# Kernel tuning notes

Measured on AMD Instinct MI355X. Metric: run time of the kernel, lower is better.

Reference implementation:

```python
import jax, jax.numpy as jnp
import numpy as np

D_MODEL = 1024
N_HEADS = 16
HEAD_DIM = D_MODEL // N_HEADS
SEQ = 2048
BATCH = 2
ROPE_BASE = 10000.0


def rope_cos_sin(seq_len, dim, dtype=jnp.float32):
    inv_freq = 1.0 / (ROPE_BASE ** (jnp.arange(0, dim, 2, dtype=jnp.float32) / dim))
    pos = jnp.arange(seq_len, dtype=jnp.float32)
    freqs = jnp.outer(pos, inv_freq)              # [S, dim/2]
    emb = jnp.concatenate([freqs, freqs], axis=-1)  # [S, dim]
    return jnp.cos(emb).astype(dtype), jnp.sin(emb).astype(dtype)


def rotate_half(x):
    x1, x2 = jnp.split(x, 2, axis=-1)
    return jnp.concatenate([-x2, x1], axis=-1)


def setup_inputs() -> dict:
    key = jax.random.key(0)
    kx, kq, kk, kv, ko = jax.random.split(key, 5)
    x = jax.random.normal(kx, (BATCH, SEQ, D_MODEL), dtype=jnp.float32)
    # causal boolean mask, broadcastable to [B, H, S, S]
    attn_mask = jnp.tril(jnp.ones((SEQ, SEQ), dtype=bool))[None, None]
    s = 1.0 / np.sqrt(D_MODEL)
    Wq = jax.random.normal(kq, (D_MODEL, D_MODEL), dtype=jnp.float32) * s
    Wk = jax.random.normal(kk, (D_MODEL, D_MODEL), dtype=jnp.float32) * s
    Wv = jax.random.normal(kv, (D_MODEL, D_MODEL), dtype=jnp.float32) * s
    Wo = jax.random.normal(ko, (D_MODEL, D_MODEL), dtype=jnp.float32) * s
    return {"x": x, "attn_mask": attn_mask, "Wq": Wq, "Wk": Wk, "Wv": Wv, "Wo": Wo}


def reference(x, attn_mask, Wq, Wk, Wv, Wo):
    B, S, _ = x.shape
    dtype = x.dtype
    # projections (nn.Linear: x @ W.T)
    def split_heads(t):
        return t.reshape(B, S, N_HEADS, HEAD_DIM).transpose(0, 2, 1, 3)  # [B,H,S,Dh]
    q = split_heads(x @ Wq.T)
    k = split_heads(x @ Wk.T)
    v = split_heads(x @ Wv.T)
    # RoPE
    cos, sin = rope_cos_sin(S, HEAD_DIM, dtype)  # [S, Dh]
    cos = cos[None, None]
    sin = sin[None, None]
    q = q * cos + rotate_half(q) * sin
    k = k * cos + rotate_half(k) * sin
    # float mask: 0 where True, finfo.min where False
    neg = jnp.finfo(dtype).min
    float_mask = jnp.where(attn_mask, jnp.zeros((), dtype), jnp.full((), neg, dtype))
    # scaled dot product attention
    scale = 1.0 / np.sqrt(HEAD_DIM)
    scores = jnp.einsum("bhqd,bhkd->bhqk", q, k) * scale + float_mask
    attn = jax.nn.softmax(scores, axis=-1)
    out = jnp.einsum("bhqk,bhkd->bhqd", attn, v)  # [B,H,S,Dh]
    out = out.transpose(0, 2, 1, 3).reshape(B, S, D_MODEL)
    return out @ Wo.T
```

## Files before the change

### kernel.cpp

```cpp
#include <hip/hip_runtime.h>
#include <hip/hip_bf16.h>
#include <math.h>

typedef unsigned short ushort_t;
typedef __attribute__((ext_vector_type(8))) short short8;
typedef __attribute__((ext_vector_type(4))) float f32x4;

#define D_MODEL 1024
#define SEQ     2048
#define NH      16
#define HD      64
#define BATCH   2
#define M_TOTAL (BATCH * SEQ)
#define SCL     0.18033688f
#define HSZ     4194304

__device__ __forceinline__ ushort_t f2bf(float f) {
    __hip_bfloat16 h = __float2bfloat16(f);
    ushort_t u;
    __builtin_memcpy(&u, &h, 2);
    return u;
}
__device__ __forceinline__ unsigned pack2(float a, float b) {
    __hip_bfloat162 h = __float22bfloat162_rn(make_float2(a, b));
    unsigned u;
    __builtin_memcpy(&u, &h, 4);
    return u;
}
__device__ __forceinline__ float fexp2(float x) { return __builtin_amdgcn_exp2f(x); }

typedef const __attribute__((address_space(1))) void* gp_t;
typedef __attribute__((address_space(3))) void* lp_t;
__device__ __forceinline__ void cp16(const void* g, void* l) {
    __builtin_amdgcn_global_load_lds((gp_t)g, (lp_t)l, 16, 0, 0);
}

__global__ __launch_bounds__(256) void prep(
    const float* __restrict__ x,
    const float* __restrict__ w0, const float* __restrict__ w1,
    const float* __restrict__ w2, const float* __restrict__ w3,
    ushort_t* __restrict__ xb, ushort_t* __restrict__ wb,
    float2* __restrict__ tab)
{
    int bid = blockIdx.x;
    if (bid < 4096) {
        size_t e = ((size_t)bid * 256 + threadIdx.x) * 8;
        const float* src;
        ushort_t* dst;
        size_t off;
        if (e < (size_t)HSZ) {
            src = x; dst = xb; off = e;
        } else {
            size_t r = e - HSZ;
            int j = (int)(r >> 20);
            off = r & 1048575u;
            src = (j == 0) ? w0 : (j == 1) ? w1 : (j == 2) ? w2 : w3;
            dst = wb + ((size_t)j << 20);
        }
        float4 a = *(const float4*)&src[off];
        float4 b = *(const float4*)&src[off + 4];
        uint4 u;
        u.x = pack2(a.x, a.y);
        u.y = pack2(a.z, a.w);
        u.z = pack2(b.x, b.y);
        u.w = pack2(b.z, b.w);
        *(uint4*)&dst[off] = u;
    } else {
        int idx = (bid - 4096) * 256 + threadIdx.x;
        int i = idx & 31, s = idx >> 5;
        float invf = powf(10000.0f, -(float)(2 * i) * (1.0f / 64.0f));
        float fr = (float)s * invf;
        float sn, cs;
        sincosf(fr, &sn, &cs);
        tab[idx] = make_float2(cs, sn);
    }
}


#define STAGE(K0, SB) do {                                                   \
    cp16(&A [(size_t)(m0 + ro0) * K + (K0) + c0 * 8], &As[SB][i0 * 8]);      \
    cp16(&A [(size_t)(m0 + ro1) * K + (K0) + c1 * 8], &As[SB][i1 * 8]);      \
    cp16(&Wp[(size_t)(n0 + ro0) * K + (K0) + c0 * 8], &Bs[SB][i0 * 8]);      \
    cp16(&Wp[(size_t)(n0 + ro1) * K + (K0) + c1 * 8], &Bs[SB][i1 * 8]);      \
} while (0)

#define K_ITER(SK0, BUF, SBUF, DOSTAGE, LAST) {                              \
    if constexpr (LAST) {                                                    \
        asm volatile("s_waitcnt vmcnt(0)" ::: "memory");                     \
    } else {                                                                 \
        asm volatile("s_waitcnt vmcnt(4)" ::: "memory");                     \
    }                                                                        \
    __builtin_amdgcn_s_barrier();                                            \
    if constexpr (DOSTAGE) { STAGE(SK0, SBUF); }                             \
    short8 af_[4], bf_[4];                                                   \
    _Pragma("unroll")                                                        \
    for (int i = 0; i < 4; ++i) {                                            \
        int R = wm + 16 * i + r15;                                           \
        af_[i] = *(const short8*)&As[BUF][(R * 4 + ((q4 + (R >> 1)) & 3)) * 8]; \
    }                                                                        \
    _Pragma("unroll")                                                        \
    for (int j = 0; j < 4; ++j) {                                            \
        int R = wn + 16 * j + r15;                                           \
        bf_[j] = *(const short8*)&Bs[BUF][(R * 4 + ((q4 + (R >> 1)) & 3)) * 8]; \
    }                                                                        \
    __builtin_amdgcn_s_setprio(1);                                           \
    _Pragma("unroll")                                                        \
    for (int i = 0; i < 4; ++i) {                                            \
        _Pragma("unroll")                                                    \
        for (int j = 0; j < 4; ++j)                                          \
            acc[i][j] = __builtin_amdgcn_mfma_f32_16x16x32_bf16(             \
                af_[i], bf_[j], acc[i][j], 0, 0, 0);                         \
    }                                                                        \
    __builtin_amdgcn_s_setprio(0);                                           \
    asm volatile("s_waitcnt lgkmcnt(0)" ::: "memory");                       \
    __builtin_amdgcn_s_barrier();                                            \
}

__global__ __launch_bounds__(256, 3) void gemm_qkv(
    const ushort_t* __restrict__ A,
    const ushort_t* __restrict__ W0, const ushort_t* __restrict__ W1,
    const ushort_t* __restrict__ W2,
    void* __restrict__ D0v, void* __restrict__ D1v, void* __restrict__ D2v,
    const float2* __restrict__ tab)
{
    __shared__ ushort_t As[3][128 * 32];
    __shared__ ushort_t Bs[3][128 * 32];
    const int K = D_MODEL;
    const int t = threadIdx.x;
    const int l = t & 63, w = t >> 6;
    const int wm = (w & 1) * 64, wn = (w >> 1) * 64;
    const int r15 = l & 15, q4 = l >> 4;

    const int bid = blockIdx.x;
    const int xcd = bid & 7, loc = bid >> 3;
    const int mt = (xcd >> 1) * 8 + (loc & 7);
    int rest = loc >> 3;
    const int nt = (xcd & 1) * 4 + (rest & 3);
    const int z  = rest >> 2;
    const int m0 = mt * 128, n0 = nt * 128;
    const ushort_t* Wp = (z == 0) ? W0 : (z == 1 ? W1 : W2);
    void* Dp           = (z == 0) ? D0v : (z == 1 ? D1v : D2v);

    f32x4 acc[4][4];
#pragma unroll
    for (int i = 0; i < 4; ++i)
#pragma unroll
        for (int j = 0; j < 4; ++j) acc[i][j] = (f32x4){0.f, 0.f, 0.f, 0.f};

    const int i0 = t, i1 = t + 256;
    const int ro0 = i0 >> 2, c0 = ((i0 & 3) - (ro0 >> 1)) & 3;
    const int ro1 = i1 >> 2, c1 = ((i1 & 3) - (ro1 >> 1)) & 3;

    STAGE(0, 0);
    STAGE(32, 1);
#pragma unroll 1
    for (int kb = 0; kb < 10; ++kb) {
        const int k6 = kb * 96;
        K_ITER(k6 + 64,  0, 2, 1, 0)
        K_ITER(k6 + 96,  1, 0, 1, 0)
        K_ITER(k6 + 128, 2, 1, 1, 0)
    }
    K_ITER(0, 0, 0, 0, 0)
    K_ITER(0, 1, 0, 0, 1)

    if (z < 2) {
        ushort_t* Dst = (ushort_t*)Dp;
        const float scl = (z == 0) ? SCL : 1.0f;
#pragma unroll
        for (int i = 0; i < 4; ++i) {
#pragma unroll
            for (int r = 0; r < 4; ++r) {
                int row = m0 + wm + 16 * i + q4 * 4 + r;
                int b = row >> 11, s = row & (SEQ - 1);
                const float2* trow = &tab[s * 32];
#pragma unroll
                for (int j = 0; j < 2; ++j) {
                    int col = n0 + wn + 16 * j + r15;
                    int h = col >> 6, f = 16 * j + r15;
                    float2 csn = trow[f];
                    float cs = csn.x * scl, sn = csn.y * scl;
                    float lo = acc[i][j][r], hi = acc[i][j + 2][r];
                    size_t o = (((size_t)(b * NH + h)) * SEQ + s) * HD + f;
                    Dst[o]      = f2bf(lo * cs - hi * sn);
                    Dst[o + 32] = f2bf(hi * cs + lo * sn);
                }
            }
        }
    } else {
        ushort_t* Dst = (ushort_t*)Dp;
#pragma unroll
        for (int i = 0; i < 4; ++i)
#pragma unroll
            for (int j = 0; j < 4; ++j) {
                int row0 = m0 + wm + 16 * i + q4 * 4;
                int col  = n0 + wn + 16 * j + r15;
                int b = row0 >> 11, s0 = row0 & (SEQ - 1);
                int h = col >> 6, d = col & (HD - 1);
                size_t o = (((size_t)(b * NH + h)) * HD + d) * SEQ + s0;
                uint2 u;
                u.x = pack2(acc[i][j][0], acc[i][j][1]);
                u.y = pack2(acc[i][j][2], acc[i][j][3]);
                *(uint2*)&Dst[o] = u;
            }
    }
}

#undef K_ITER
#undef STAGE


#define STAGE_O(K0, SB) do {                                                 \
    cp16(&A [(size_t)(m0 + roa0) * K + (K0) + ca0 * 8], &As[SB][ia0 * 8]);   \
    cp16(&A [(size_t)(m0 + roa1) * K + (K0) + ca1 * 8], &As[SB][ia1 * 8]);   \
    cp16(&A [(size_t)(m0 + roa2) * K + (K0) + ca2 * 8], &As[SB][ia2 * 8]);   \
    cp16(&A [(size_t)(m0 + roa3) * K + (K0) + ca3 * 8], &As[SB][ia3 * 8]);   \
    cp16(&Wp[(size_t)(n0 + rob0) * K + (K0) + cb0 * 8], &Bs[SB][ib0 * 8]);   \
    cp16(&Wp[(size_t)(n0 + rob1) * K + (K0) + cb1 * 8], &Bs[SB][ib1 * 8]);   \
} while (0)

#define K_ITER_O(SK0, BUF, SBUF, DOSTAGE, LAST) {                            \
    if constexpr (LAST) {                                                    \
        asm volatile("s_waitcnt vmcnt(0)" ::: "memory");                     \
    } else {                                                                 \
        asm volatile("s_waitcnt vmcnt(6)" ::: "memory");                     \
    }                                                                        \
    __builtin_amdgcn_s_barrier();                                            \
    if constexpr (DOSTAGE) { STAGE_O(SK0, SBUF); }                           \
    short8 af_[4][2], bf_[2][2];                                             \
    _Pragma("unroll")                                                        \
    for (int i = 0; i < 4; ++i) {                                            \
        int R = wm + 16 * i + r15;                                           \
        _Pragma("unroll")                                                    \
        for (int kk = 0; kk < 2; ++kk)                                       \
            af_[i][kk] = *(const short8*)                                    \
                &As[BUF][(R * 8 + ((kk * 4 + q4) ^ (R & 7))) * 8];           \
    }                                                                        \
    _Pragma("unroll")                                                        \
    for (int j = 0; j < 2; ++j) {                                            \
        int R = wn + 16 * j + r15;                                           \
        _Pragma("unroll")                                                    \
        for (int kk = 0; kk < 2; ++kk)                                       \
            bf_[j][kk] = *(const short8*)                                    \
                &Bs[BUF][(R * 8 + ((kk * 4 + q4) ^ (R & 7))) * 8];           \
    }                                                                        \
    __builtin_amdgcn_s_setprio(1);                                           \
    _Pragma("unroll")                                                        \
    for (int kk = 0; kk < 2; ++kk) {                                         \
        _Pragma("unroll")                                                    \
        for (int i = 0; i < 4; ++i) {                                        \
            _Pragma("unroll")                                                \
            for (int j = 0; j < 2; ++j)                                      \
                acc[i][j] = __builtin_amdgcn_mfma_f32_16x16x32_bf16(         \
                    af_[i][kk], bf_[j][kk], acc[i][j], 0, 0, 0);             \
        }                                                                    \
    }                                                                        \
    __builtin_amdgcn_s_setprio(0);                                           \
    asm volatile("s_waitcnt lgkmcnt(0)" ::: "memory");                       \
    __builtin_amdgcn_s_barrier();                                            \
}

__global__ __launch_bounds__(256, 2) void gemm_o(
    const ushort_t* __restrict__ A, const ushort_t* __restrict__ Wp,
    float* __restrict__ Dst)
{
    __shared__ ushort_t As[3][128 * 64];
    __shared__ ushort_t Bs[3][64 * 64];
    const int K = D_MODEL;
    const int t = threadIdx.x;
    const int l = t & 63, w = t >> 6;
    const int wm = (w & 1) * 64, wn = (w >> 1) * 32;
    const int r15 = l & 15, q4 = l >> 4;

    const int bid = blockIdx.x;
    const int xcd = bid & 7, loc = bid >> 3;
    const int mt = (xcd >> 1) * 8 + (loc & 7);
    const int nt = (xcd & 1) * 8 + (loc >> 3);
    const int m0 = mt * 128, n0 = nt * 64;

    f32x4 acc[4][2];
#pragma unroll
    for (int i = 0; i < 4; ++i)
#pragma unroll
        for (int j = 0; j < 2; ++j) acc[i][j] = (f32x4){0.f, 0.f, 0.f, 0.f};

    const int ia0 = t,       roa0 = ia0 >> 3, ca0 = (ia0 & 7) ^ (roa0 & 7);
    const int ia1 = t + 256, roa1 = ia1 >> 3, ca1 = (ia1 & 7) ^ (roa1 & 7);
    const int ia2 = t + 512, roa2 = ia2 >> 3, ca2 = (ia2 & 7) ^ (roa2 & 7);
    const int ia3 = t + 768, roa3 = ia3 >> 3, ca3 = (ia3 & 7) ^ (roa3 & 7);
    const int ib0 = t,       rob0 = ib0 >> 3, cb0 = (ib0 & 7) ^ (rob0 & 7);
    const int ib1 = t + 256, rob1 = ib1 >> 3, cb1 = (ib1 & 7) ^ (rob1 & 7);

    STAGE_O(0, 0);
    STAGE_O(64, 1);
#pragma unroll 1
    for (int kb = 0; kb < 4; ++kb) {
        const int k6 = kb * 192;
        K_ITER_O(k6 + 128, 0, 2, 1, 0)
        K_ITER_O(k6 + 192, 1, 0, 1, 0)
        K_ITER_O(k6 + 256, 2, 1, 1, 0)
    }
    K_ITER_O(896, 0, 2, 1, 0)
    K_ITER_O(960, 1, 0, 1, 0)
    K_ITER_O(0,   2, 0, 0, 0)
    K_ITER_O(0,   0, 0, 0, 1)

#pragma unroll
    for (int i = 0; i < 4; ++i)
#pragma unroll
        for (int j = 0; j < 2; ++j)
#pragma unroll
            for (int r = 0; r < 4; ++r) {
                int row = m0 + wm + 16 * i + q4 * 4 + r;
                int col = n0 + wn + 16 * j + r15;
                Dst[(size_t)row * D_MODEL + col] = acc[i][j][r];
            }
}

#undef K_ITER_O
#undef STAGE_O

__global__ __launch_bounds__(256, 2) void attn_fused(
    const ushort_t* __restrict__ Qw, const ushort_t* __restrict__ Kw,
    const ushort_t* __restrict__ Vt, ushort_t* __restrict__ Ow)
{
    __shared__ __align__(16) ushort_t Kl[2][64 * 64];
    __shared__ __align__(16) ushort_t Vl[2][64 * 64];
    __shared__ __align__(16) ushort_t Ps[4][32 * 72];

    const int t = threadIdx.x;
    const int l = t & 63, w = t >> 6;
    const int r15 = l & 15, q4 = l >> 4;
    const int bid = blockIdx.x;
    const int xcd = bid & 7, loc = bid >> 3;
    const int p   = loc >> 1, e = loc & 1;
    const int head_l = p >> 3, u = p & 7;
    const int T   = e ? u : (15 - u);
    const int bh  = xcd * 4 + head_l;
    const int B0  = T * 128;
    const int NT  = 2 * T + 2;
    const int rb0 = B0 + 32 * w;
    const int wtop = rb0 >> 6;
    const size_t baseQK = (size_t)bh * SEQ * HD;
    const size_t baseV  = (size_t)bh * HD * SEQ;

    const int L0 = t, L1 = t + 256;
    const int r0 = L0 >> 3, c0 = (L0 & 7) ^ (r0 & 7);
    const int r1 = L1 >> 3, c1 = (L1 & 7) ^ (r1 & 7);

    short8 qf[2][2];
#pragma unroll
    for (int s = 0; s < 2; ++s) {
        const ushort_t* qp =
            &Qw[baseQK + (size_t)(rb0 + 16 * s + r15) * HD + q4 * 8];
        qf[s][0] = *(const short8*)qp;
        qf[s][1] = *(const short8*)(qp + 32);
    }

    f32x4 oacc[2][4];
    float part[2][4];
#pragma unroll
    for (int s = 0; s < 2; ++s)
#pragma unroll
        for (int nb = 0; nb < 4; ++nb) {
            oacc[s][nb] = (f32x4){0.f, 0.f, 0.f, 0.f};
            part[s][nb] = 0.f;
        }

    ushort_t* ps = &Ps[w][0];

    auto stage = [&](int jt, int buf) {
        cp16(&Kw[baseQK + (size_t)(jt * 64 + r0) * HD + c0 * 8], &Kl[buf][L0 * 8]);
        cp16(&Kw[baseQK + (size_t)(jt * 64 + r1) * HD + c1 * 8], &Kl[buf][L1 * 8]);
        cp16(&Vt[baseV + (size_t)r0 * SEQ + jt * 64 + c0 * 8],   &Vl[buf][L0 * 8]);
        cp16(&Vt[baseV + (size_t)r1 * SEQ + jt * 64 + c1 * 8],   &Vl[buf][L1 * 8]);
    };

    auto process = [&](int jt, int buf) {
        f32x4 sc[2][4];
#pragma unroll
        for (int nb = 0; nb < 4; ++nb) {
            int R  = nb * 16 + r15;
            int a0 = R * 8 + (q4 ^ (R & 7));
            int a1 = R * 8 + ((q4 + 4) ^ (R & 7));
            short8 kb0 = *(const short8*)&Kl[buf][a0 * 8];
            short8 kb1 = *(const short8*)&Kl[buf][a1 * 8];
#pragma unroll
            for (int s = 0; s < 2; ++s) {
                f32x4 zz = (f32x4){0.f, 0.f, 0.f, 0.f};
                zz = __builtin_amdgcn_mfma_f32_16x16x32_bf16(qf[s][0], kb0, zz, 0, 0, 0);
                sc[s][nb] = __builtin_amdgcn_mfma_f32_16x16x32_bf16(qf[s][1], kb1, zz, 0, 0, 0);
            }
        }
        const bool diag = (jt == wtop);
#pragma unroll
        for (int s = 0; s < 2; ++s) {
            const int ig0 = rb0 + 16 * s + q4 * 4;
#pragma unroll
            for (int r = 0; r < 4; ++r) {
                float p0 = fexp2(sc[s][0][r]), p1 = fexp2(sc[s][1][r]);
                float p2 = fexp2(sc[s][2][r]), p3 = fexp2(sc[s][3][r]);
                if (diag) {
                    int qg = ig0 + r, jb = jt * 64 + r15;
                    p0 = (jb      <= qg) ? p0 : 0.f;
                    p1 = (jb + 16 <= qg) ? p1 : 0.f;
                    p2 = (jb + 32 <= qg) ? p2 : 0.f;
                    p3 = (jb + 48 <= qg) ? p3 : 0.f;
                }
                part[s][r] += (p0 + p1) + (p2 + p3);
                int ro = (s * 16 + q4 * 4 + r) * 72 + r15;
                ps[ro]      = f2bf(p0);
                ps[ro + 16] = f2bf(p1);
                ps[ro + 32] = f2bf(p2);
                ps[ro + 48] = f2bf(p3);
            }
        }
        short8 pf[2][2];
#pragma unroll
        for (int s = 0; s < 2; ++s) {
            pf[s][0] = *(const short8*)&ps[(s * 16 + r15) * 72 + q4 * 8];
            pf[s][1] = *(const short8*)&ps[(s * 16 + r15) * 72 + q4 * 8 + 32];
        }
#pragma unroll
        for (int nb = 0; nb < 4; ++nb) {
            int R  = nb * 16 + r15;
            int a0 = R * 8 + (q4 ^ (R & 7));
            int a1 = R * 8 + ((q4 + 4) ^ (R & 7));
            short8 vb0 = *(const short8*)&Vl[buf][a0 * 8];
            short8 vb1 = *(const short8*)&Vl[buf][a1 * 8];
#pragma unroll
            for (int s = 0; s < 2; ++s) {
                f32x4 o = __builtin_amdgcn_mfma_f32_16x16x32_bf16(pf[s][0], vb0, oacc[s][nb], 0, 0, 0);
                oacc[s][nb] = __builtin_amdgcn_mfma_f32_16x16x32_bf16(pf[s][1], vb1, o, 0, 0, 0);
            }
        }
    };

    stage(0, 0);
    for (int jt = 0; jt < NT; ++jt) {
        __syncthreads();
        if (jt < NT - 1) stage(jt + 1, (jt + 1) & 1);
        if (jt <= wtop) process(jt, jt & 1);
    }

    const int b = bh >> 4, h = bh & 15;
#pragma unroll
    for (int s = 0; s < 2; ++s) {
        float lsum[4];
#pragma unroll
        for (int r = 0; r < 4; ++r) {
            float rs = part[s][r];
#pragma unroll
            for (int off = 1; off < 16; off <<= 1)
                rs += __shfl_xor(rs, off, 64);
            lsum[r] = 1.0f / rs;
        }
#pragma unroll
        for (int nb = 0; nb < 4; ++nb) {
#pragma unroll
            for (int r = 0; r < 4; ++r) {
                int sg = rb0 + 16 * s + q4 * 4 + r;
                int d  = nb * 16 + r15;
                Ow[((size_t)(b * SEQ + sg)) * D_MODEL + h * HD + d] =
                    f2bf(oacc[s][nb][r] * lsum[r]);
            }
        }
    }
}

extern "C" void kernel_launch(void* const* d_in, const int* in_sizes, int n_in,
                              void* d_out, int out_size, void* d_ws, size_t ws_size,
                              hipStream_t stream)
{
    const float* x  = (const float*)d_in[0];
    const float* Wq = (const float*)d_in[2];
    const float* Wk = (const float*)d_in[3];
    const float* Wv = (const float*)d_in[4];
    const float* Wo = (const float*)d_in[5];

    ushort_t* qw = (ushort_t*)d_ws;
    ushort_t* kw = qw + HSZ;
    ushort_t* vt = kw + HSZ;
    ushort_t* xb = vt + HSZ;
    ushort_t* aw = xb;
    ushort_t* wb = xb + HSZ;
    float2*  tab = (float2*)(wb + HSZ);

    prep<<<4096 + 256, 256, 0, stream>>>(x, Wq, Wk, Wv, Wo, xb, wb, tab);
    gemm_qkv<<<768, 256, 0, stream>>>(
        xb, wb, wb + (1 << 20), wb + (2 << 20), qw, kw, vt, tab);
    attn_fused<<<512, 256, 0, stream>>>(qw, kw, vt, aw);
    gemm_o<<<512, 256, 0, stream>>>(aw, wb + (3 << 20), (float*)d_out);
}
```

Baseline: 201.5 us.

## Split attention KV range across two blocks and combine partials

Each query tile's key range is split into two halves handled by separate blocks, doubling the grid to 1024 blocks. Unnormalized fp32 outputs and row sums go to workspace, and a new combine kernel adds them, normalizes and writes the bf16 attention output. Launch bounds rise to 3 blocks per CU. The aim is better load balance and occupancy on the causal workload, at the cost of extra global traffic, an extra launch, and possible register pressure. The split appears to skip a running max, so summing the two halves' partials is only valid if both use the same fixed shift.

```diff
diff --git a/kernel.cpp b/kernel.cpp
--- a/kernel.cpp
+++ b/kernel.cpp
@@ -14,6 +14,7 @@
 #define M_TOTAL (BATCH * SEQ)
 #define SCL     0.18033688f
 #define HSZ     4194304
+#define NROWS   65536
 
 __device__ __forceinline__ ushort_t f2bf(float f) {
     __hip_bfloat16 h = __float2bfloat16(f);
@@ -319,9 +320,10 @@
 #undef K_ITER_O
 #undef STAGE_O
 
-__global__ __launch_bounds__(256, 2) void attn_fused(
+__global__ __launch_bounds__(256, 3) void attn_fused(
     const ushort_t* __restrict__ Qw, const ushort_t* __restrict__ Kw,
-    const ushort_t* __restrict__ Vt, ushort_t* __restrict__ Ow)
+    const ushort_t* __restrict__ Vt,
+    float* __restrict__ Po, float* __restrict__ Psum)
 {
     __shared__ __align__(16) ushort_t Kl[2][64 * 64];
     __shared__ __align__(16) ushort_t Vl[2][64 * 64];
@@ -332,14 +334,14 @@
     const int r15 = l & 15, q4 = l >> 4;
     const int bid = blockIdx.x;
     const int xcd = bid & 7, loc = bid >> 3;
-    const int p   = loc >> 1, e = loc & 1;
-    const int head_l = p >> 3, u = p & 7;
-    const int T   = e ? u : (15 - u);
-    const int bh  = xcd * 4 + head_l;
-    const int B0  = T * 128;
-    const int NT  = 2 * T + 2;
-    const int rb0 = B0 + 32 * w;
+    const int bh  = xcd * 4 + (loc & 3);
+    const int v   = loc >> 2;
+    const int T   = 15 - (v >> 1);
+    const int half = v & 1;
+    const int rb0 = T * 128 + 32 * w;
     const int wtop = rb0 >> 6;
+    const int jtS = half ? (T + 1) : 0;
+    const int jtE = half ? (2 * T + 2) : (T + 1);
     const size_t baseQK = (size_t)bh * SEQ * HD;
     const size_t baseV  = (size_t)bh * HD * SEQ;
 
@@ -435,24 +437,24 @@
         }
     };
 
-    stage(0, 0);
-    for (int jt = 0; jt < NT; ++jt) {
+    stage(jtS, 0);
+    for (int jt = jtS; jt < jtE; ++jt) {
         __syncthreads();
-        if (jt < NT - 1) stage(jt + 1, (jt + 1) & 1);
-        if (jt <= wtop) process(jt, jt & 1);
-    }
-
-    const int b = bh >> 4, h = bh & 15;
+        if (jt + 1 < jtE) stage(jt + 1, (jt + 1 - jtS) & 1);
+        if (jt <= wtop) process(jt, (jt - jtS) & 1);
+    }
+
+    const size_t rowbase = (size_t)half * NROWS + (size_t)bh * SEQ;
 #pragma unroll
     for (int s = 0; s < 2; ++s) {
-        float lsum[4];
 #pragma unroll
         for (int r = 0; r < 4; ++r) {
             float rs = part[s][r];
 #pragma unroll
             for (int off = 1; off < 16; off <<= 1)
                 rs += __shfl_xor(rs, off, 64);
-            lsum[r] = 1.0f / rs;
+            if (r15 == 0)
+                Psum[rowbase + rb0 + 16 * s + q4 * 4 + r] = rs;
         }
 #pragma unroll
         for (int nb = 0; nb < 4; ++nb) {
@@ -460,11 +462,31 @@
             for (int r = 0; r < 4; ++r) {
                 int sg = rb0 + 16 * s + q4 * 4 + r;
                 int d  = nb * 16 + r15;
-                Ow[((size_t)(b * SEQ + sg)) * D_MODEL + h * HD + d] =
-                    f2bf(oacc[s][nb][r] * lsum[r]);
-            }
-        }
-    }
+                Po[(rowbase + sg) * HD + d] = oacc[s][nb][r];
+            }
+        }
+    }
+}
+
+__global__ __launch_bounds__(256) void combine(
+    const float* __restrict__ Po, const float* __restrict__ Psum,
+    ushort_t* __restrict__ Ow)
+{
+    int idx = blockIdx.x * 256 + threadIdx.x;
+    int row = idx >> 3;
+    int d0  = (idx & 7) << 3;
+    float inv = 1.0f / (Psum[row] + Psum[NROWS + row]);
+    const float4* a = (const float4*)&Po[(size_t)row * HD + d0];
+    const float4* c = (const float4*)&Po[((size_t)NROWS + row) * HD + d0];
+    float4 x0 = a[0], x1 = a[1], y0 = c[0], y1 = c[1];
+    uint4 u;
+    u.x = pack2((x0.x + y0.x) * inv, (x0.y + y0.y) * inv);
+    u.y = pack2((x0.z + y0.z) * inv, (x0.w + y0.w) * inv);
+    u.z = pack2((x1.x + y1.x) * inv, (x1.y + y1.y) * inv);
+    u.w = pack2((x1.z + y1.z) * inv, (x1.w + y1.w) * inv);
+    int bh = row >> 11, sg = row & (SEQ - 1);
+    int b = bh >> 4, h = bh & 15;
+    *(uint4*)&Ow[(((size_t)(b * SEQ + sg)) << 10) + h * HD + d0] = u;
 }
 
 extern "C" void kernel_launch(void* const* d_in, const int* in_sizes, int n_in,
@@ -484,10 +506,13 @@
     ushort_t* aw = xb;
     ushort_t* wb = xb + HSZ;
     float2*  tab = (float2*)(wb + HSZ);
+    float*    po = (float*)(tab + 65536);
+    float*   psb = po + 2ll * NROWS * HD;
 
     prep<<<4096 + 256, 256, 0, stream>>>(x, Wq, Wk, Wv, Wo, xb, wb, tab);
     gemm_qkv<<<768, 256, 0, stream>>>(
         xb, wb, wb + (1 << 20), wb + (2 << 20), qw, kw, vt, tab);
-    attn_fused<<<512, 256, 0, stream>>>(qw, kw, vt, aw);
+    attn_fused<<<1024, 256, 0, stream>>>(qw, kw, vt, po, psb);
+    combine<<<2048, 256, 0, stream>>>(po, psb, aw);
     gemm_o<<<512, 256, 0, stream>>>(aw, wb + (3 << 20), (float*)d_out);
 }
```

Result: faster. 186.2 us (-7.6%).
